# Kernel tuning notes

Measured on AMD Instinct MI355X. Metric: run time of the kernel, lower is better.

## Reference

```python
import jax, jax.numpy as jnp
import numpy as np

N, E, IN, HID, HEADS, OUT, G = 30000, 480000, 256, 64, 8, 128, 512
NEG_SLOPE = 0.2


def setup_inputs() -> dict:
    key = jax.random.key(0)
    ks = jax.random.split(key, 20)
    def nrm(k, shape, scale=0.05):
        return jax.random.normal(k, shape, dtype=jnp.float32) * scale
    inp = {
        'x': jax.random.normal(ks[0], (N, IN), dtype=jnp.float32),
        'edge_index': jax.random.randint(ks[1], (2, E), 0, N, dtype=jnp.int32),
        'batch': jnp.sort(jax.random.randint(ks[2], (N,), 0, G, dtype=jnp.int32)),
        # conv1: in=IN, out=HID, heads=HEADS (concat)
        'W1': nrm(ks[3], (IN, HEADS * HID)),
        'a_src1': nrm(ks[4], (HEADS, HID)),
        'a_dst1': nrm(ks[5], (HEADS, HID)),
        'b1': jnp.zeros((HEADS * HID,), jnp.float32),
        # conv2: in=HEADS*HID, out=HID, heads=HEADS (concat)
        'W2': nrm(ks[6], (HEADS * HID, HEADS * HID)),
        'a_src2': nrm(ks[7], (HEADS, HID)),
        'a_dst2': nrm(ks[8], (HEADS, HID)),
        'b2': jnp.zeros((HEADS * HID,), jnp.float32),
        # conv3: in=HEADS*HID, out=HID, heads=1
        'W3': nrm(ks[9], (HEADS * HID, HID)),
        'a_src3': nrm(ks[10], (1, HID)),
        'a_dst3': nrm(ks[11], (1, HID)),
        'b3': jnp.zeros((HID,), jnp.float32),
        # fc
        'Wfc': nrm(ks[12], (HID, OUT)),
        'bfc': jnp.zeros((OUT,), jnp.float32),
    }
    return inp


def gat_conv(x, W, a_src, a_dst, b, src, dst, heads, ch):
    # x: [N, in] -> h: [N, heads, ch]
    h = (x @ W).reshape(N, heads, ch)
    alpha_s = jnp.einsum('nhc,hc->nh', h, a_src)  # [N,H]
    alpha_d = jnp.einsum('nhc,hc->nh', h, a_dst)
    e = jax.nn.leaky_relu(alpha_s[src] + alpha_d[dst], NEG_SLOPE)  # [E',H]
    # segment softmax over incoming edges of each dst node
    e = e - jax.ops.segment_max(e, dst, num_segments=N)[dst]
    e = jnp.exp(e)
    alpha = e / jax.ops.segment_sum(e, dst, num_segments=N)[dst]
    msg = h[src] * alpha[:, :, None]                   # [E',H,C]
    out = jax.ops.segment_sum(msg, dst, num_segments=N)  # [N,H,C]
    return out.reshape(N, heads * ch) + b


def reference(x, edge_index, batch, W1, a_src1, a_dst1, b1, W2, a_src2, a_dst2, b2,
              W3, a_src3, a_dst3, b3, Wfc, bfc):
    # PyG GATConv adds self-loops
    loops = jnp.arange(N, dtype=edge_index.dtype)
    src = jnp.concatenate([edge_index[0], loops])
    dst = jnp.concatenate([edge_index[1], loops])

    h = jax.nn.elu(gat_conv(x, W1, a_src1, a_dst1, b1, src, dst, HEADS, HID))
    h = jax.nn.elu(gat_conv(h, W2, a_src2, a_dst2, b2, src, dst, HEADS, HID))
    h = jax.nn.elu(gat_conv(h, W3, a_src3, a_dst3, b3, src, dst, 1, HID))

    # global mean pool over graphs
    sums = jax.ops.segment_sum(h, batch, num_segments=G)          # [G,HID]
    cnt = jax.ops.segment_sum(jnp.ones((N,), h.dtype), batch, num_segments=G)
    pooled = sums / jnp.maximum(cnt, 1.0)[:, None]
    # dropout(p=0.5) is identity in eval mode
    return pooled @ Wfc + bfc  # [G, OUT]
```

## Files before the change

### kernel.cpp

```cpp
#include <hip/hip_runtime.h>
#include <hip/hip_fp16.h>
#include <math.h>

#define N_NODES 30000
#define N_EDGES 480000
#define N_EDGES_SL (N_EDGES + N_NODES)
#define CSRC_CAP (N_EDGES + 4 * N_NODES)
#define DIM_IN 256
#define F1 512
#define HEADS 8
#define NGRAPH 512
#define NEG 0.2f
#define MB_TILES 235
#define NB_SCAN 118

typedef __attribute__((ext_vector_type(8))) short short8;
typedef __attribute__((ext_vector_type(8))) _Float16 half8;
typedef __attribute__((ext_vector_type(4))) float f32x4;

__device__ __forceinline__ float lrelu(float x) { return fmaxf(x, NEG * x); }
__device__ __forceinline__ float elu_(float x) { return x > 0.f ? x : __expf(x) - 1.f; }

__device__ __forceinline__ void glds16(const unsigned short* g, unsigned short* l) {
    __builtin_amdgcn_global_load_lds(
        (const __attribute__((address_space(1))) unsigned int*)g,
        (__attribute__((address_space(3))) unsigned int*)l, 16, 0, 0);
}

__device__ __forceinline__ int plen_of(int deg) { return (deg + 4) & ~3; }

__global__ __launch_bounds__(256) void k_bsum(const int* __restrict__ deg,
                                              int* __restrict__ bsum) {
    int i = blockIdx.x * 256 + threadIdx.x;
    int v = (i < N_NODES) ? plen_of(deg[i]) : 0;
#pragma unroll
    for (int off = 1; off < 64; off <<= 1) v += __shfl_xor(v, off);
    __shared__ int ws[4];
    if ((threadIdx.x & 63) == 0) ws[threadIdx.x >> 6] = v;
    __syncthreads();
    if (threadIdx.x == 0) bsum[blockIdx.x] = ws[0] + ws[1] + ws[2] + ws[3];
}

__global__ __launch_bounds__(128) void k_bscan(const int* __restrict__ bsum,
                                               int* __restrict__ bbase,
                                               int* __restrict__ offsN) {
    __shared__ int p[128];
    int t = threadIdx.x;
    int v = (t < NB_SCAN) ? bsum[t] : 0;
    p[t] = v;
    __syncthreads();
    for (int off = 1; off < 128; off <<= 1) {
        int x = (t >= off) ? p[t - off] : 0;
        __syncthreads();
        p[t] += x;
        __syncthreads();
    }
    if (t < NB_SCAN) bbase[t] = p[t] - v;
    if (t == 127) *offsN = p[127];
}

__global__ __launch_bounds__(256) void k_offs(const int* __restrict__ deg,
                                              const int* __restrict__ bbase,
                                              int* __restrict__ offs,
                                              int* __restrict__ cursor,
                                              unsigned short* __restrict__ csrc) {
    int b = blockIdx.x, t = threadIdx.x;
    int i = b * 256 + t;
    int d1 = 0, v = 0;
    if (i < N_NODES) { d1 = deg[i] + 1; v = (d1 + 3) & ~3; }
    __shared__ int p[256];
    p[t] = v;
    __syncthreads();
    for (int off = 1; off < 256; off <<= 1) {
        int x = (t >= off) ? p[t - off] : 0;
        __syncthreads();
        p[t] += x;
        __syncthreads();
    }
    if (i < N_NODES) {
        int excl = bbase[b] + p[t] - v;
        offs[i] = excl | (v - d1);
        cursor[i] = excl;
        for (int pp = excl + d1; pp < excl + v; ++pp) csrc[pp] = 0;
    }
}

__global__ void k_scatter(const int* __restrict__ ei, int* __restrict__ cursor,
                          unsigned short* __restrict__ csrc) {
    int i = blockIdx.x * blockDim.x + threadIdx.x;
    if (i >= N_EDGES_SL) return;
    int s, d;
    if (i < N_EDGES) { s = ei[i]; d = ei[N_EDGES + i]; }
    else { s = d = i - N_EDGES; }
    int p = atomicAdd(&cursor[d], 1);
    csrc[p] = (unsigned short)s;
}

__device__ __forceinline__ void d_packA(int t, const float* __restrict__ A,
                                        unsigned short* __restrict__ out,
                                        int M, int K) {
    int KB = K >> 5;
    int k8 = t & 3;
    int ml = (t >> 2) & 127;
    int tmp = t >> 9;
    int kb = tmp % KB;
    int mb = tmp / KB;
    int m = mb * 128 + ml;
    int k0 = kb * 32 + k8 * 8;
    float v[8] = {0.f, 0.f, 0.f, 0.f, 0.f, 0.f, 0.f, 0.f};
    if (m < M) {
        float4 p0 = *(const float4*)(A + (size_t)m * K + k0);
        float4 p1 = *(const float4*)(A + (size_t)m * K + k0 + 4);
        v[0] = p0.x; v[1] = p0.y; v[2] = p0.z; v[3] = p0.w;
        v[4] = p1.x; v[5] = p1.y; v[6] = p1.z; v[7] = p1.w;
    }
    unsigned short h[8];
#pragma unroll
    for (int j = 0; j < 8; ++j) h[j] = __half_as_ushort(__float2half(v[j]));
    *(short8*)(out + (size_t)t * 8) = *(short8*)h;
}

__device__ __forceinline__ void d_packW(int t, const float* __restrict__ W,
                                        unsigned short* __restrict__ out,
                                        int K, int Nn, int BN, int LB) {
    int KB = K >> 5;
    int k8 = t & 3;
    int tmp = t >> 2;
    int nl = tmp & (BN - 1);
    int tmp2 = tmp >> LB;
    int kb = tmp2 % KB;
    int nb = tmp2 / KB;
    int n = nb * BN + nl;
    int k0 = kb * 32 + k8 * 8;
    unsigned short h[8];
#pragma unroll
    for (int j = 0; j < 8; ++j)
        h[j] = __half_as_ushort(__float2half(W[(size_t)(k0 + j) * Nn + n]));
    *(short8*)(out + (size_t)t * 8) = *(short8*)h;
}

#define PB_A 3760
#define PB_W1 64
#define PB_W2 128
#define PB_W3 16
#define PB_B 118
#define PB_CNT 1875
__global__ __launch_bounds__(256) void k_packall(
        const float* __restrict__ x, const float* __restrict__ W1,
        const float* __restrict__ W2, const float* __restrict__ W3,
        const int* __restrict__ batch, const int* __restrict__ ei,
        unsigned short* __restrict__ Ah,
        unsigned short* __restrict__ Wh1, unsigned short* __restrict__ Wh2,
        unsigned short* __restrict__ Wh3, int* __restrict__ gstart,
        int* __restrict__ deg) {
    int b = blockIdx.x, tid = threadIdx.x;
    if (b < PB_A) {
        d_packA(b * 256 + tid, x, Ah, N_NODES, DIM_IN);
    } else if (b < PB_A + PB_W1) {
        d_packW((b - PB_A) * 256 + tid, W1, Wh1, DIM_IN, F1, 128, 7);
    } else if (b < PB_A + PB_W1 + PB_W2) {
        d_packW((b - PB_A - PB_W1) * 256 + tid, W2, Wh2, F1, F1, 128, 7);
    } else if (b < PB_A + PB_W1 + PB_W2 + PB_W3) {
        d_packW((b - PB_A - PB_W1 - PB_W2) * 256 + tid, W3, Wh3, F1, 64, 64, 6);
    } else if (b < PB_A + PB_W1 + PB_W2 + PB_W3 + PB_B) {
        int bb = b - (PB_A + PB_W1 + PB_W2 + PB_W3);
        int i = bb * 256 + tid;
        if (i >= N_NODES) return;
        int bt = batch[i];
        int pb = (i == 0) ? -1 : batch[i - 1];
        for (int g = pb + 1; g <= bt; ++g) gstart[g] = i;
        if (i == N_NODES - 1)
            for (int g = bt + 1; g <= NGRAPH; ++g) gstart[g] = N_NODES;
    } else {
        int i = (b - (PB_A + PB_W1 + PB_W2 + PB_W3 + PB_B)) * 256 + tid;
        if (i < N_EDGES) atomicAdd(&deg[ei[N_EDGES + i]], 1);
    }
}
#define PACKALL_BLOCKS (PB_A + PB_W1 + PB_W2 + PB_W3 + PB_B + PB_CNT)

template <int KB>
__global__ __launch_bounds__(256) void k_gemm8(const unsigned short* __restrict__ Ah,
                                               const unsigned short* __restrict__ Bh,
                                               const float* __restrict__ a_src,
                                               const float* __restrict__ a_dst,
                                               __half* __restrict__ Hf,
                                               float* __restrict__ as_,
                                               float* __restrict__ ad_,
                                               int M) {
    __shared__ unsigned short sA[4096], sB[4096];
    const int tid = threadIdx.x, lane = tid & 63, wave = tid >> 6;
    const int mb = blockIdx.x, nb = blockIdx.y;
    const int wm = (wave >> 1) * 64;
    const int wn = (wave & 1) * 64;
    const int fr = lane & 15, quad = lane >> 4;

    const unsigned short* pA = Ah + (size_t)mb * KB * 4096;
    const unsigned short* pB = Bh + (size_t)nb * KB * 4096;

    f32x4 acc[4][4];
#pragma unroll
    for (int i = 0; i < 4; ++i)
#pragma unroll
        for (int j = 0; j < 4; ++j) acc[i][j] = {0.f, 0.f, 0.f, 0.f};

    for (int kb = 0; kb < KB; ++kb) {
        const unsigned short* a_g = pA + kb * 4096;
        const unsigned short* b_g = pB + kb * 4096;
#pragma unroll
        for (int s = 0; s < 2; ++s) {
            int sg = wave * 2 + s;
            glds16(a_g + sg * 512 + lane * 8, &sA[sg * 512]);
            glds16(b_g + sg * 512 + lane * 8, &sB[sg * 512]);
        }
        __syncthreads();

        half8 af[4], bf[4];
#pragma unroll
        for (int f = 0; f < 4; ++f) {
            int m = wm + f * 16 + fr;
            af[f] = *(const half8*)&sA[m * 32 + quad * 8];
            int n = wn + f * 16 + fr;
            bf[f] = *(const half8*)&sB[n * 32 + quad * 8];
        }
#pragma unroll
        for (int i = 0; i < 4; ++i)
#pragma unroll
            for (int j = 0; j < 4; ++j)
                acc[i][j] = __builtin_amdgcn_mfma_f32_16x16x32_f16(af[i], bf[j], acc[i][j], 0, 0, 0);
        __syncthreads();
    }
    const int head = (nb * 128 + wn) >> 6;
    float avs[4], avd[4];
#pragma unroll
    for (int j = 0; j < 4; ++j) {
        avs[j] = a_src[head * 64 + j * 16 + fr];
        avd[j] = a_dst[head * 64 + j * 16 + fr];
    }
    __half* Hh = Hf + (size_t)head * N_NODES * 64;
#pragma unroll
    for (int i = 0; i < 4; ++i) {
#pragma unroll
        for (int r = 0; r < 4; ++r) {
            int row = mb * 128 + wm + i * 16 + quad * 4 + r;
            bool ok = row < M;
            float vs = 0.f, vd = 0.f;
#pragma unroll
            for (int j = 0; j < 4; ++j) {
                float c = acc[i][j][r];
                vs = fmaf(c, avs[j], vs);
                vd = fmaf(c, avd[j], vd);
                if (ok) Hh[(size_t)row * 64 + j * 16 + fr] = __float2half(c);
            }
#pragma unroll
            for (int off = 1; off < 16; off <<= 1) {
                vs += __shfl_xor(vs, off);
                vd += __shfl_xor(vd, off);
            }
            if (ok && fr == 0) {
                as_[head * N_NODES + row] = vs;
                ad_[head * N_NODES + row] = vd;
            }
        }
    }
}

template <int KB>
__global__ __launch_bounds__(256) void k_gemm1(const unsigned short* __restrict__ Ah,
                                               const unsigned short* __restrict__ Bh,
                                               const float* __restrict__ a_src,
                                               const float* __restrict__ a_dst,
                                               __half* __restrict__ C,
                                               float* __restrict__ as_,
                                               float* __restrict__ ad_,
                                               int M) {
    __shared__ unsigned short sA[4096], sB[2048];
    const int tid = threadIdx.x, lane = tid & 63, wave = tid >> 6;
    const int mb = blockIdx.x;
    const int wm = (wave >> 1) * 64;
    const int wn = (wave & 1) * 32;
    const int fr = lane & 15, quad = lane >> 4;

    const unsigned short* pA = Ah + (size_t)mb * KB * 4096;

    f32x4 acc[4][2];
#pragma unroll
    for (int i = 0; i < 4; ++i)
#pragma unroll
        for (int j = 0; j < 2; ++j) acc[i][j] = {0.f, 0.f, 0.f, 0.f};

    for (int kb = 0; kb < KB; ++kb) {
        const unsigned short* a_g = pA + kb * 4096;
        const unsigned short* b_g = Bh + kb * 2048;
#pragma unroll
        for (int s = 0; s < 2; ++s) {
            int sg = wave * 2 + s;
            glds16(a_g + sg * 512 + lane * 8, &sA[sg * 512]);
        }
        glds16(b_g + wave * 512 + lane * 8, &sB[wave * 512]);
        __syncthreads();

        half8 af[4], bf[2];
#pragma unroll
        for (int f = 0; f < 4; ++f) {
            int m = wm + f * 16 + fr;
            af[f] = *(const half8*)&sA[m * 32 + quad * 8];
        }
#pragma unroll
        for (int f = 0; f < 2; ++f) {
            int n = wn + f * 16 + fr;
            bf[f] = *(const half8*)&sB[n * 32 + quad * 8];
        }
#pragma unroll
        for (int i = 0; i < 4; ++i)
#pragma unroll
            for (int j = 0; j < 2; ++j)
                acc[i][j] = __builtin_amdgcn_mfma_f32_16x16x32_f16(af[i], bf[j], acc[i][j], 0, 0, 0);
        __syncthreads();
    }
    float avs[2], avd[2];
#pragma unroll
    for (int j = 0; j < 2; ++j) {
        avs[j] = a_src[wn + j * 16 + fr];
        avd[j] = a_dst[wn + j * 16 + fr];
    }
    float* ps = (float*)sA;
    float* pd = (float*)sB;
#pragma unroll
    for (int i = 0; i < 4; ++i) {
#pragma unroll
        for (int r = 0; r < 4; ++r) {
            int rl = wm + i * 16 + quad * 4 + r;
            int row = mb * 128 + rl;
            bool ok = row < M;
            float vs = 0.f, vd = 0.f;
#pragma unroll
            for (int j = 0; j < 2; ++j) {
                float c = acc[i][j][r];
                vs = fmaf(c, avs[j], vs);
                vd = fmaf(c, avd[j], vd);
                if (ok) C[(size_t)row * 64 + wn + j * 16 + fr] = __float2half(c);
            }
#pragma unroll
            for (int off = 1; off < 16; off <<= 1) {
                vs += __shfl_xor(vs, off);
                vd += __shfl_xor(vd, off);
            }
            if (fr == 0) {
                ps[wave * 64 + (rl & 63)] = vs;
                pd[wave * 64 + (rl & 63)] = vd;
            }
        }
    }
    __syncthreads();
    if (tid < 128) {
        int row = mb * 128 + tid;
        if (row < M) {
            int wp = (tid >> 6) * 2;
            as_[row] = ps[wp * 64 + (tid & 63)] + ps[(wp + 1) * 64 + (tid & 63)];
            ad_[row] = pd[wp * 64 + (tid & 63)] + pd[(wp + 1) * 64 + (tid & 63)];
        }
    }
}

__device__ __forceinline__ void edge_fma(float w, uint4 u, float* a) {
    const _Float16* hp = (const _Float16*)&u;
#pragma unroll
    for (int k = 0; k < 8; ++k) a[k] = fmaf(w, (float)hp[k], a[k]);
}

__global__ __launch_bounds__(256) void k_agg8(const __half* __restrict__ Hf,
                                              const float* __restrict__ as_,
                                              const float* __restrict__ ad_,
                                              const int* __restrict__ offs,
                                              const unsigned short* __restrict__ csrc,
                                              const float* __restrict__ bias,
                                              unsigned short* __restrict__ outA) {
    const int head = blockIdx.x & 7;
    const int bg = blockIdx.x >> 3;
    const int wave = threadIdx.x >> 6, lane = threadIdx.x & 63;
    const int g = lane >> 3, cl = lane & 7;
    const unsigned coff = (unsigned)(cl * 8);
    const __half* Hh = Hf + (size_t)head * N_NODES * 64;
    const float* ash = as_ + head * N_NODES;
    const float* adh = ad_ + head * N_NODES;

    int d0 = (bg * 4 + wave) * 8;
    if (d0 >= N_NODES) return;
    int dst = d0 + g;

    float bia[8];
#pragma unroll
    for (int j = 0; j < 8; ++j) bia[j] = bias[head * 64 + cl * 8 + j];

    int raw0 = offs[dst], raw1 = offs[dst + 1];
    int beg = raw0 & ~3;
    int plen = (raw1 & ~3) - beg;
    int nreal = 4 - (raw0 & 3);
    float adv = adh[dst];
    const unsigned short* cp = csrc + beg;

    float s = 0.f;
    float a[8] = {0.f, 0.f, 0.f, 0.f, 0.f, 0.f, 0.f, 0.f};
    float b[8] = {0.f, 0.f, 0.f, 0.f, 0.f, 0.f, 0.f, 0.f};
    ushort4 idx = *(const ushort4*)cp;
    int loc = 0;
    for (; loc < plen - 4; loc += 4) {
        unsigned i0 = idx.x, i1 = idx.y, i2 = idx.z, i3 = idx.w;
        float e0 = ash[i0], e1 = ash[i1], e2 = ash[i2], e3 = ash[i3];
        uint4 u0 = *(const uint4*)(Hh + i0 * 64u + coff);
        uint4 u1 = *(const uint4*)(Hh + i1 * 64u + coff);
        uint4 u2 = *(const uint4*)(Hh + i2 * 64u + coff);
        uint4 u3 = *(const uint4*)(Hh + i3 * 64u + coff);
        idx = *(const ushort4*)(cp + loc + 4);
        float w0 = __expf(lrelu(e0 + adv));
        float w1 = __expf(lrelu(e1 + adv));
        float w2 = __expf(lrelu(e2 + adv));
        float w3 = __expf(lrelu(e3 + adv));
        s += (w0 + w1) + (w2 + w3);
        edge_fma(w0, u0, a);
        edge_fma(w1, u1, b);
        edge_fma(w2, u2, a);
        edge_fma(w3, u3, b);
    }
    {
        unsigned i0 = idx.x, i1 = idx.y, i2 = idx.z, i3 = idx.w;
        float e0 = ash[i0], e1 = ash[i1], e2 = ash[i2], e3 = ash[i3];
        uint4 u0 = *(const uint4*)(Hh + i0 * 64u + coff);
        uint4 u1 = *(const uint4*)(Hh + i1 * 64u + coff);
        uint4 u2 = *(const uint4*)(Hh + i2 * 64u + coff);
        uint4 u3 = *(const uint4*)(Hh + i3 * 64u + coff);
        float w0 = __expf(lrelu(e0 + adv));
        float w1 = (nreal > 1) ? __expf(lrelu(e1 + adv)) : 0.f;
        float w2 = (nreal > 2) ? __expf(lrelu(e2 + adv)) : 0.f;
        float w3 = (nreal > 3) ? __expf(lrelu(e3 + adv)) : 0.f;
        s += (w0 + w1) + (w2 + w3);
        edge_fma(w0, u0, a);
        edge_fma(w1, u1, b);
        edge_fma(w2, u2, a);
        edge_fma(w3, u3, b);
    }
    float inv = 1.f / s;
    unsigned short h[8];
#pragma unroll
    for (int k = 0; k < 8; ++k)
        h[k] = __half_as_ushort(__float2half(elu_((a[k] + b[k]) * inv + bia[k])));
    int c0 = head * 64 + cl * 8;
    int kb = c0 >> 5, kl = c0 & 31;
    int mb = dst >> 7, ml = dst & 127;
    size_t oo = (((size_t)(mb * 16 + kb) * 128 + ml) * 32 + kl);
    *(short8*)(outA + oo) = *(short8*)h;
}

__global__ __launch_bounds__(256) void k_agg1(const __half* __restrict__ Hf,
                                              const float* __restrict__ as_,
                                              const float* __restrict__ ad_,
                                              const int* __restrict__ offs,
                                              const unsigned short* __restrict__ csrc,
                                              const float* __restrict__ bias,
                                              float* __restrict__ h3) {
    const int wave = threadIdx.x >> 6, lane = threadIdx.x & 63;
    const int g = lane >> 3, cl = lane & 7;
    const unsigned coff = (unsigned)(cl * 8);
    int d0 = (blockIdx.x * 4 + wave) * 8;
    if (d0 >= N_NODES) return;
    int dst = d0 + g;
    float bia[8];
#pragma unroll
    for (int j = 0; j < 8; ++j) bia[j] = bias[cl * 8 + j];

    int raw0 = offs[dst], raw1 = offs[dst + 1];
    int beg = raw0 & ~3;
    int plen = (raw1 & ~3) - beg;
    int nreal = 4 - (raw0 & 3);
    float adv = ad_[dst];
    const unsigned short* cp = csrc + beg;

    float s = 0.f;
    float a[8] = {0.f, 0.f, 0.f, 0.f, 0.f, 0.f, 0.f, 0.f};
    float b[8] = {0.f, 0.f, 0.f, 0.f, 0.f, 0.f, 0.f, 0.f};
    ushort4 idx = *(const ushort4*)cp;
    int loc = 0;
    for (; loc < plen - 4; loc += 4) {
        unsigned i0 = idx.x, i1 = idx.y, i2 = idx.z, i3 = idx.w;
        float e0 = as_[i0], e1 = as_[i1], e2 = as_[i2], e3 = as_[i3];
        uint4 u0 = *(const uint4*)(Hf + i0 * 64u + coff);
        uint4 u1 = *(const uint4*)(Hf + i1 * 64u + coff);
        uint4 u2 = *(const uint4*)(Hf + i2 * 64u + coff);
        uint4 u3 = *(const uint4*)(Hf + i3 * 64u + coff);
        idx = *(const ushort4*)(cp + loc + 4);
        float w0 = __expf(lrelu(e0 + adv));
        float w1 = __expf(lrelu(e1 + adv));
        float w2 = __expf(lrelu(e2 + adv));
        float w3 = __expf(lrelu(e3 + adv));
        s += (w0 + w1) + (w2 + w3);
        edge_fma(w0, u0, a);
        edge_fma(w1, u1, b);
        edge_fma(w2, u2, a);
        edge_fma(w3, u3, b);
    }
    {
        unsigned i0 = idx.x, i1 = idx.y, i2 = idx.z, i3 = idx.w;
        float e0 = as_[i0], e1 = as_[i1], e2 = as_[i2], e3 = as_[i3];
        uint4 u0 = *(const uint4*)(Hf + i0 * 64u + coff);
        uint4 u1 = *(const uint4*)(Hf + i1 * 64u + coff);
        uint4 u2 = *(const uint4*)(Hf + i2 * 64u + coff);
        uint4 u3 = *(const uint4*)(Hf + i3 * 64u + coff);
        float w0 = __expf(lrelu(e0 + adv));
        float w1 = (nreal > 1) ? __expf(lrelu(e1 + adv)) : 0.f;
        float w2 = (nreal > 2) ? __expf(lrelu(e2 + adv)) : 0.f;
        float w3 = (nreal > 3) ? __expf(lrelu(e3 + adv)) : 0.f;
        s += (w0 + w1) + (w2 + w3);
        edge_fma(w0, u0, a);
        edge_fma(w1, u1, b);
        edge_fma(w2, u2, a);
        edge_fma(w3, u3, b);
    }
    float inv = 1.f / s;
    float o[8];
#pragma unroll
    for (int k = 0; k < 8; ++k) o[k] = elu_((a[k] + b[k]) * inv + bia[k]);
    float* op = h3 + (size_t)dst * 64 + cl * 8;
    *(float4*)op = make_float4(o[0], o[1], o[2], o[3]);
    *(float4*)(op + 4) = make_float4(o[4], o[5], o[6], o[7]);
}

__global__ __launch_bounds__(128) void k_poolfc(const float* __restrict__ h3,
                                                const int* __restrict__ gstart,
                                                const float* __restrict__ W,
                                                const float* __restrict__ b,
                                                float* __restrict__ out) {
    int g = blockIdx.x;
    int t = threadIdx.x;
    int s0 = gstart[g], s1 = gstart[g + 1];
    int c = t & 63, half = t >> 6;
    float acc = 0.f;
    for (int r = s0 + half; r < s1; r += 2) acc += h3[(size_t)r * 64 + c];
    __shared__ float p2[128];
    __shared__ float p[64];
    p2[t] = acc;
    __syncthreads();
    if (t < 64) {
        float cntf = (float)(s1 - s0);
        p[t] = (p2[t] + p2[t + 64]) / fmaxf(cntf, 1.f);
    }
    __syncthreads();
    float o = b[t];
#pragma unroll
    for (int k = 0; k < 64; ++k) o = fmaf(p[k], W[k * 128 + t], o);
    out[g * 128 + t] = o;
}

extern "C" void kernel_launch(void* const* d_in, const int* in_sizes, int n_in,
                              void* d_out, int out_size, void* d_ws, size_t ws_size,
                              hipStream_t stream) {
    const float* x     = (const float*)d_in[0];
    const int*   ei    = (const int*)d_in[1];
    const int*   batch = (const int*)d_in[2];
    const float* W1    = (const float*)d_in[3];
    const float* as1   = (const float*)d_in[4];
    const float* ad1   = (const float*)d_in[5];
    const float* b1    = (const float*)d_in[6];
    const float* W2    = (const float*)d_in[7];
    const float* as2   = (const float*)d_in[8];
    const float* ad2   = (const float*)d_in[9];
    const float* b2    = (const float*)d_in[10];
    const float* W3    = (const float*)d_in[11];
    const float* as3   = (const float*)d_in[12];
    const float* ad3   = (const float*)d_in[13];
    const float* b3    = (const float*)d_in[14];
    const float* Wfc   = (const float*)d_in[15];
    const float* bfc   = (const float*)d_in[16];
    float* out = (float*)d_out;

    char* ws = (char*)d_ws;
    size_t off = 0;
    auto alloc = [&](size_t bytes) -> void* {
        void* p = ws + off;
        off += (bytes + 255) & ~(size_t)255;
        return p;
    };
    __half* Hf = (__half*)alloc((size_t)HEADS * N_NODES * 64 * 2);
    __half* Hf3 = (__half*)alloc((size_t)N_NODES * 64 * 2);
    float* h3 = (float*)alloc((size_t)N_NODES * 64 * 4);
    unsigned short* Ah = (unsigned short*)alloc((size_t)MB_TILES * 16 * 4096 * 2);
    unsigned short* Wh1 = (unsigned short*)alloc((size_t)131072 * 2);
    unsigned short* Wh2 = (unsigned short*)alloc((size_t)262144 * 2);
    unsigned short* Wh3 = (unsigned short*)alloc((size_t)32768 * 2);
    float* asb   = (float*)alloc((size_t)HEADS * N_NODES * 4);
    float* adb   = (float*)alloc((size_t)HEADS * N_NODES * 4);
    int*   offs  = (int*)alloc((N_NODES + 1) * 4);
    int*   deg   = (int*)alloc(N_NODES * 4);
    int*   cursor= (int*)alloc(N_NODES * 4);
    unsigned short* csrc = (unsigned short*)alloc((size_t)CSRC_CAP * 2 + 64);
    int*   bsum  = (int*)alloc(NB_SCAN * 4);
    int*   bbase = (int*)alloc(NB_SCAN * 4);
    int*   gstart= (int*)alloc((NGRAPH + 1) * 4);

    hipMemsetAsync(deg, 0, N_NODES * 4, stream);

    k_packall<<<PACKALL_BLOCKS, 256, 0, stream>>>(x, W1, W2, W3, batch, ei, Ah,
                                                  Wh1, Wh2, Wh3, gstart, deg);
    k_bsum<<<NB_SCAN, 256, 0, stream>>>(deg, bsum);
    k_bscan<<<1, 128, 0, stream>>>(bsum, bbase, offs + N_NODES);
    k_offs<<<NB_SCAN, 256, 0, stream>>>(deg, bbase, offs, cursor, csrc);
    k_scatter<<<(N_EDGES_SL + 255) / 256, 256, 0, stream>>>(ei, cursor, csrc);

    k_gemm8<8><<<dim3(MB_TILES, 4), 256, 0, stream>>>(Ah, Wh1, as1, ad1, Hf, asb, adb, N_NODES);
    k_agg8<<<938 * 8, 256, 0, stream>>>(Hf, asb, adb, offs, csrc, b1, Ah);

    k_gemm8<16><<<dim3(MB_TILES, 4), 256, 0, stream>>>(Ah, Wh2, as2, ad2, Hf, asb, adb, N_NODES);
    k_agg8<<<938 * 8, 256, 0, stream>>>(Hf, asb, adb, offs, csrc, b2, Ah);

    k_gemm1<16><<<MB_TILES, 256, 0, stream>>>(Ah, Wh3, as3, ad3, Hf3, asb, adb, N_NODES);
    k_agg1<<<940, 256, 0, stream>>>(Hf3, asb, adb, offs, csrc, b3, h3);

    k_poolfc<<<NGRAPH, 128, 0, stream>>>(h3, gstart, Wfc, bfc, out);
}
```

Baseline: 355.5 us.

## Sort destination nodes by degree to balance wavefront work in aggregation

Builds a degree histogram, scans it, and produces a permutation of destination nodes bucketed by padded in-degree. The aggregation kernels then process nodes in this order, so the 8 nodes sharing a wavefront have similar edge counts and lanes diverge less. This adds three small kernels plus a memset, an indirect perm lookup per node, and scattered output writes instead of contiguous ones. Node order within a bin is nondeterministic because of the atomics, but results are unaffected.

```diff
diff --git a/kernel.cpp b/kernel.cpp
--- a/kernel.cpp
+++ b/kernel.cpp
@@ -30,9 +30,15 @@
 __device__ __forceinline__ int plen_of(int deg) { return (deg + 4) & ~3; }
 
 __global__ __launch_bounds__(256) void k_bsum(const int* __restrict__ deg,
-                                              int* __restrict__ bsum) {
+                                              int* __restrict__ bsum,
+                                              int* __restrict__ hist) {
     int i = blockIdx.x * 256 + threadIdx.x;
-    int v = (i < N_NODES) ? plen_of(deg[i]) : 0;
+    int v = 0;
+    if (i < N_NODES) {
+        v = plen_of(deg[i]);
+        int bin = min(v >> 2, 255);
+        atomicAdd(&hist[bin], 1);
+    }
 #pragma unroll
     for (int off = 1; off < 64; off <<= 1) v += __shfl_xor(v, off);
     __shared__ int ws[4];
@@ -57,6 +63,32 @@
     }
     if (t < NB_SCAN) bbase[t] = p[t] - v;
     if (t == 127) *offsN = p[127];
+}
+
+__global__ __launch_bounds__(256) void k_hscan(const int* __restrict__ hist,
+                                               int* __restrict__ hbase) {
+    __shared__ int p[256];
+    int t = threadIdx.x;
+    int v = hist[t];
+    p[t] = v;
+    __syncthreads();
+    for (int off = 1; off < 256; off <<= 1) {
+        int x = (t >= off) ? p[t - off] : 0;
+        __syncthreads();
+        p[t] += x;
+        __syncthreads();
+    }
+    hbase[t] = p[t] - v;
+}
+
+__global__ __launch_bounds__(256) void k_perm(const int* __restrict__ deg,
+                                              int* __restrict__ hbase,
+                                              int* __restrict__ perm) {
+    int i = blockIdx.x * 256 + threadIdx.x;
+    if (i >= N_NODES) return;
+    int bin = min((deg[i] + 4) >> 2, 255);
+    int pos = atomicAdd(&hbase[bin], 1);
+    perm[pos] = i;
 }
 
 __global__ __launch_bounds__(256) void k_offs(const int* __restrict__ deg,
@@ -373,6 +405,7 @@
                                               const float* __restrict__ ad_,
                                               const int* __restrict__ offs,
                                               const unsigned short* __restrict__ csrc,
+                                              const int* __restrict__ perm,
                                               const float* __restrict__ bias,
                                               unsigned short* __restrict__ outA) {
     const int head = blockIdx.x & 7;
@@ -386,7 +419,7 @@
 
     int d0 = (bg * 4 + wave) * 8;
     if (d0 >= N_NODES) return;
-    int dst = d0 + g;
+    int dst = perm[d0 + g];
 
     float bia[8];
 #pragma unroll
@@ -456,6 +489,7 @@
                                               const float* __restrict__ ad_,
                                               const int* __restrict__ offs,
                                               const unsigned short* __restrict__ csrc,
+                                              const int* __restrict__ perm,
                                               const float* __restrict__ bias,
                                               float* __restrict__ h3) {
     const int wave = threadIdx.x >> 6, lane = threadIdx.x & 63;
@@ -463,7 +497,7 @@
     const unsigned coff = (unsigned)(cl * 8);
     int d0 = (blockIdx.x * 4 + wave) * 8;
     if (d0 >= N_NODES) return;
-    int dst = d0 + g;
+    int dst = perm[d0 + g];
     float bia[8];
 #pragma unroll
     for (int j = 0; j < 8; ++j) bia[j] = bias[cl * 8 + j];
@@ -595,24 +629,30 @@
     int*   bsum  = (int*)alloc(NB_SCAN * 4);
     int*   bbase = (int*)alloc(NB_SCAN * 4);
     int*   gstart= (int*)alloc((NGRAPH + 1) * 4);
+    int*   hist  = (int*)alloc(256 * 4);
+    int*   hbase = (int*)alloc(256 * 4);
+    int*   perm  = (int*)alloc(N_NODES * 4);
 
     hipMemsetAsync(deg, 0, N_NODES * 4, stream);
+    hipMemsetAsync(hist, 0, 256 * 4, stream);
 
     k_packall<<<PACKALL_BLOCKS, 256, 0, stream>>>(x, W1, W2, W3, batch, ei, Ah,
                                                   Wh1, Wh2, Wh3, gstart, deg);
-    k_bsum<<<NB_SCAN, 256, 0, stream>>>(deg, bsum);
+    k_bsum<<<NB_SCAN, 256, 0, stream>>>(deg, bsum, hist);
     k_bscan<<<1, 128, 0, stream>>>(bsum, bbase, offs + N_NODES);
+    k_hscan<<<1, 256, 0, stream>>>(hist, hbase);
     k_offs<<<NB_SCAN, 256, 0, stream>>>(deg, bbase, offs, cursor, csrc);
+    k_perm<<<NB_SCAN, 256, 0, stream>>>(deg, hbase, perm);
     k_scatter<<<(N_EDGES_SL + 255) / 256, 256, 0, stream>>>(ei, cursor, csrc);
 
     k_gemm8<8><<<dim3(MB_TILES, 4), 256, 0, stream>>>(Ah, Wh1, as1, ad1, Hf, asb, adb, N_NODES);
-    k_agg8<<<938 * 8, 256, 0, stream>>>(Hf, asb, adb, offs, csrc, b1, Ah);
+    k_agg8<<<938 * 8, 256, 0, stream>>>(Hf, asb, adb, offs, csrc, perm, b1, Ah);
 
     k_gemm8<16><<<dim3(MB_TILES, 4), 256, 0, stream>>>(Ah, Wh2, as2, ad2, Hf, asb, adb, N_NODES);
-    k_agg8<<<938 * 8, 256, 0, stream>>>(Hf, asb, adb, offs, csrc, b2, Ah);
+    k_agg8<<<938 * 8, 256, 0, stream>>>(Hf, asb, adb, offs, csrc, perm, b2, Ah);
 
     k_gemm1<16><<<MB_TILES, 256, 0, stream>>>(Ah, Wh3, as3, ad3, Hf3, asb, adb, N_NODES);
-    k_agg1<<<940, 256, 0, stream>>>(Hf3, asb, adb, offs, csrc, b3, h3);
+    k_agg1<<<940, 256, 0, stream>>>(Hf3, asb, adb, offs, csrc, perm, b3, h3);
 
     k_poolfc<<<NGRAPH, 128, 0, stream>>>(h3, gstart, Wfc, bfc, out);
 }
```

New measurement: 709.1 us. +99.5%, slower.
